# Kernel tuning notes

Hardware: AMD Instinct MI355X
Metric: run time of the kernel (lower is better)

## Reference

```python
import jax, jax.numpy as jnp
import numpy as np

BN_EPS = 1e-5
L2_EPS = 1e-12


def setup_inputs() -> dict:
    key = jax.random.key(0)
    k1, k2, k3 = jax.random.split(key, 3)
    B, N, D, K, G = 32, 2048, 512, 64, 16
    init_sc = 1.0 / np.sqrt(D)
    x = jax.random.normal(k1, (B, N, D), dtype=jnp.float32)
    clusters = init_sc * jax.random.normal(k2, (D, K + G), dtype=jnp.float32)
    clusters2 = init_sc * jax.random.normal(k3, (1, D, K), dtype=jnp.float32)
    bn_gamma = jnp.ones((K + G,), dtype=jnp.float32)
    bn_beta = jnp.zeros((K + G,), dtype=jnp.float32)
    return {"x": x, "clusters": clusters, "clusters2": clusters2,
            "bn_gamma": bn_gamma, "bn_beta": bn_beta}


def reference(x, clusters, clusters2, bn_gamma, bn_beta):
    B, N, D = x.shape
    K = clusters2.shape[-1]
    xf = x.reshape(B * N, D)
    # soft cluster assignment: [B*N, K+G]
    assn = xf @ clusters
    # BatchNorm1d (training-mode batch statistics, biased variance)
    mean = jnp.mean(assn, axis=0)
    var = jnp.var(assn, axis=0)
    assn = (assn - mean) * jax.lax.rsqrt(var + BN_EPS) * bn_gamma + bn_beta
    # softmax over clusters, then drop ghost clusters
    assn = jax.nn.softmax(assn, axis=1)[:, :K].reshape(B, N, K)
    # residual aggregation
    a_sum = jnp.sum(assn, axis=1, keepdims=True)          # [B, 1, K]
    a = a_sum * clusters2                                  # [B, D, K]
    vlad = jnp.einsum("bnk,bnd->bdk", assn, x) - a         # [B, D, K]
    # intra-normalization across feature dim D
    vlad = vlad / jnp.maximum(jnp.linalg.norm(vlad, axis=1, keepdims=True), L2_EPS)
    # flatten and global L2 normalization
    vlad = vlad.reshape(B, D * K)
    vlad = vlad / jnp.maximum(jnp.linalg.norm(vlad, axis=1, keepdims=True), L2_EPS)
    return vlad
```

## Files before the change

kernel.cpp:

```cpp
#include <hip/hip_runtime.h>
#include <hip/hip_bf16.h>
#include <stdint.h>

typedef __attribute__((ext_vector_type(8))) short short8;
typedef __attribute__((ext_vector_type(4))) float f32x4;

__device__ __forceinline__ float b2f(uint16_t u) {
  union { uint32_t i; float f; } v; v.i = ((uint32_t)u) << 16; return v.f;
}
__device__ __forceinline__ uint16_t f2b(float f) {
  uint32_t u = __float_as_uint(f);
  return (uint16_t)((u + 0x7FFFu + ((u >> 16) & 1u)) >> 16);
}
__device__ __forceinline__ uint32_t pk2(uint32_t lo, uint32_t hi) {
  return __builtin_amdgcn_perm(hi + 0x8000u, lo + 0x8000u, 0x07060302u);
}

__global__ void k0_prep(const float* __restrict__ clusters,
                        uint16_t* __restrict__ cB) {
  int gid = blockIdx.x * 256 + threadIdx.x;
  if (gid < 40960) {
    int i = gid & 7, chunk = gid >> 3;
    int lr = chunk & 15, q = (chunk >> 4) & 3, c5 = chunk >> 6;
    int n = c5 % 5, kk = c5 / 5;
    cB[gid] = f2b(clusters[(kk * 32 + q * 8 + i) * 80 + n * 16 + lr]);
  }
}

__global__ __launch_bounds__(256) void k1_gemm1(
    const float* __restrict__ x, const uint16_t* __restrict__ cB,
    float* __restrict__ raw, float* __restrict__ part) {
  __shared__ float sf[1280];
  const int t = threadIdx.x;
  const int w = t >> 6, lane = t & 63, q = lane >> 4, lr = lane & 15;
  const int rbase = blockIdx.x * 128 + w * 32;

  f32x4 acc[2][5];
#pragma unroll
  for (int m = 0; m < 2; ++m)
#pragma unroll
    for (int n = 0; n < 5; ++n) acc[m][n] = 0.f;

  const float* xa = x + (size_t)(rbase + lr) * 512 + q * 8;
  const short8* cbq = (const short8*)cB + q * 16 + lr;

#pragma unroll 2
  for (int kk = 0; kk < 16; ++kk) {
    short8 a[2], bf[5];
#pragma unroll
    for (int m = 0; m < 2; ++m) {
      uint4 u0 = *(const uint4*)(xa + (size_t)m * 16 * 512 + kk * 32);
      uint4 u1 = *(const uint4*)(xa + (size_t)m * 16 * 512 + kk * 32 + 4);
      union { short8 s; uint32_t u[4]; } av;
      av.u[0] = pk2(u0.x, u0.y); av.u[1] = pk2(u0.z, u0.w);
      av.u[2] = pk2(u1.x, u1.y); av.u[3] = pk2(u1.z, u1.w);
      a[m] = av.s;
    }
#pragma unroll
    for (int n = 0; n < 5; ++n)
      bf[n] = cbq[(kk * 5 + n) * 64];
#pragma unroll
    for (int m = 0; m < 2; ++m)
#pragma unroll
      for (int n = 0; n < 5; ++n)
        acc[m][n] = __builtin_amdgcn_mfma_f32_16x16x32_bf16(a[m], bf[n], acc[m][n], 0, 0, 0);
  }

  float sums[5], sqs[5];
#pragma unroll
  for (int n = 0; n < 5; ++n) {
    float s = 0.f, qq = 0.f;
#pragma unroll
    for (int m = 0; m < 2; ++m) {
#pragma unroll
      for (int r = 0; r < 4; ++r) {
        float v = acc[m][n][r];
        s += v; qq += v * v;
        raw[(size_t)(rbase + m * 16 + q * 4 + r) * 80 + n * 16 + lr] = v;
      }
    }
    s += __shfl_xor(s, 16);  s += __shfl_xor(s, 32);
    qq += __shfl_xor(qq, 16); qq += __shfl_xor(qq, 32);
    sums[n] = s; sqs[n] = qq;
  }

  if (lane < 16) {
#pragma unroll
    for (int n = 0; n < 5; ++n) {
      sf[w * 160 + n * 16 + lr] = sums[n];
      sf[640 + w * 160 + n * 16 + lr] = sqs[n];
    }
  }
  __syncthreads();
  if (t < 160) {
    float a0 = sf[t] + sf[160 + t] + sf[320 + t] + sf[480 + t];
    float b0 = sf[640 + t] + sf[800 + t] + sf[960 + t] + sf[1120 + t];
    part[(size_t)t * 512 + blockIdx.x] = a0;
    part[(size_t)(160 + t) * 512 + blockIdx.x] = b0;
  }
}

__global__ __launch_bounds__(64) void k2_stats(
    const float* __restrict__ part, const float* __restrict__ gamma,
    const float* __restrict__ beta, float* __restrict__ scsh) {
  int c = blockIdx.x, t = threadIdx.x;
  const float* p1 = part + (size_t)c * 512;
  const float* p2 = part + (size_t)(160 + c) * 512;
  float s1 = 0.f, s2 = 0.f;
#pragma unroll
  for (int p = 0; p < 512; p += 64) { s1 += p1[p + t]; s2 += p2[p + t]; }
#pragma unroll
  for (int o = 1; o < 64; o <<= 1) { s1 += __shfl_xor(s1, o); s2 += __shfl_xor(s2, o); }
  if (t == 0) {
    float mean = s1 * (1.f / 65536.f);
    float var = s2 * (1.f / 65536.f) - mean * mean;
    float sc = rsqrtf(var + 1e-5f) * gamma[c];
    scsh[c] = sc;
    scsh[80 + c] = beta[c] - mean * sc;
  }
}

__global__ __launch_bounds__(256, 2) void k34_fused(
    const float* __restrict__ x, const float* __restrict__ raw_,
    const float* __restrict__ scsh, float* __restrict__ vpart,
    float* __restrict__ apart) {
  __shared__ __align__(16) uint16_t sx[2][256 * 40];
  __shared__ __align__(16) uint16_t sp[2][64 * 40];
  __shared__ float sc[80], sh[80];
  __shared__ float ared[4 * 64];

  const int t = threadIdx.x;
  const int b = blockIdx.x >> 4;
  const int s = (blockIdx.x >> 1) & 7;
  const int dh = blockIdx.x & 1;
  const int w = t >> 6, lane = t & 63, q = lane >> 4, lr = lane & 15;

  const int dd = t;
  const int sg = ((dd >> 2) + (dd >> 4)) & 3;
  const int r_ = t >> 3, cg = t & 7;
  const int kk_ = t & 63, ng = t >> 6;

  if (t < 80) sc[t] = scsh[t];
  else if (t < 160) sh[t - 80] = scsh[t];

  const float* xb = x + ((size_t)b * 2048 + (size_t)s * 256) * 512 + dh * 256;
  const float* rawb = raw_ + ((size_t)b * 2048 + (size_t)s * 256) * 80;

  f32x4 acc[4][4];
#pragma unroll
  for (int m = 0; m < 4; ++m)
#pragma unroll
    for (int j = 0; j < 4; ++j) acc[m][j] = 0.f;

  float xf[32], yf[10];
  float asum = 0.f;

#define XLOAD(c)                                                          \
  {                                                                       \
    const float* xc = xb + (size_t)(c) * 32 * 512 + dd;                   \
    _Pragma("unroll")                                                     \
    for (int j = 0; j < 32; ++j) xf[j] = xc[(size_t)j * 512];             \
  }
#define RLOAD(c)                                                          \
  {                                                                       \
    const float* rc = rawb + (size_t)((c) * 32 + r_) * 80 + cg * 10;      \
    _Pragma("unroll")                                                     \
    for (int j = 0; j < 5; ++j) {                                         \
      float2 v2 = *(const float2*)(rc + j * 2);                           \
      yf[2 * j] = v2.x; yf[2 * j + 1] = v2.y;                             \
    }                                                                     \
  }
#define XSTORE(buf)                                                       \
  {                                                                       \
    _Pragma("unroll")                                                     \
    for (int g = 0; g < 4; ++g) {                                         \
      union { uint4 u; uint32_t w4[4]; } pv;                              \
      _Pragma("unroll")                                                   \
      for (int h = 0; h < 4; ++h)                                         \
        pv.w4[h] = pk2(__float_as_uint(xf[g * 8 + h * 2]),                \
                       __float_as_uint(xf[g * 8 + h * 2 + 1]));           \
      *(uint4*)&sx[buf][dd * 40 + ((g ^ sg) << 3)] = pv.u;                \
    }                                                                     \
  }
#define SOFTMAX(buf)                                                      \
  {                                                                       \
    float yy[10]; float mx = -3.0e38f;                                    \
    _Pragma("unroll")                                                     \
    for (int j = 0; j < 10; ++j) {                                        \
      int cc = cg * 10 + j;                                               \
      yy[j] = yf[j] * sc[cc] + sh[cc];                                    \
      mx = fmaxf(mx, yy[j]);                                              \
    }                                                                     \
    mx = fmaxf(mx, __shfl_xor(mx, 1));                                    \
    mx = fmaxf(mx, __shfl_xor(mx, 2));                                    \
    mx = fmaxf(mx, __shfl_xor(mx, 4));                                    \
    float sum = 0.f;                                                      \
    _Pragma("unroll")                                                     \
    for (int j = 0; j < 10; ++j) { yy[j] = __expf(yy[j] - mx); sum += yy[j]; } \
    sum += __shfl_xor(sum, 1);                                            \
    sum += __shfl_xor(sum, 2);                                            \
    sum += __shfl_xor(sum, 4);                                            \
    float inv = 1.0f / sum;                                               \
    _Pragma("unroll")                                                     \
    for (int j = 0; j < 10; ++j) {                                        \
      int cc = cg * 10 + j;                                               \
      if (cc < 64) sp[buf][cc * 40 + r_] = f2b(yy[j] * inv);              \
    }                                                                     \
  }
#define GEMM(buf)                                                         \
  {                                                                       \
    const uint16_t* sxc = sx[buf];                                        \
    const uint16_t* spc = sp[buf];                                        \
    short8 bfr[4];                                                        \
    _Pragma("unroll")                                                     \
    for (int j = 0; j < 4; ++j)                                           \
      bfr[j] = *(const short8*)&spc[(j * 16 + lr) * 40 + (q << 3)];       \
    _Pragma("unroll")                                                     \
    for (int m = 0; m < 4; ++m) {                                         \
      int row = w * 64 + m * 16 + lr;                                     \
      int swr = ((row >> 2) + (row >> 4)) & 3;                            \
      short8 af = *(const short8*)&sxc[row * 40 + ((q ^ swr) << 3)];      \
      _Pragma("unroll")                                                   \
      for (int j = 0; j < 4; ++j)                                         \
        acc[m][j] = __builtin_amdgcn_mfma_f32_16x16x32_bf16(af, bfr[j], acc[m][j], 0, 0, 0); \
    }                                                                     \
    union { uint4 u; uint16_t us[8]; } pv;                                \
    pv.u = *(const uint4*)&spc[kk_ * 40 + (ng << 3)];                     \
    _Pragma("unroll")                                                     \
    for (int i = 0; i < 8; ++i) asum += b2f(pv.us[i]);                    \
  }

  XLOAD(0) RLOAD(0)
  __syncthreads();
  XSTORE(0) SOFTMAX(0)
  XLOAD(1) RLOAD(1)
  __syncthreads();

  for (int c = 0; c < 8; ++c) {
    const int cur = c & 1;
    if (c < 7) {
      XSTORE(cur ^ 1) SOFTMAX(cur ^ 1)
      if (c < 6) { XLOAD(c + 2) RLOAD(c + 2) }
    }
    GEMM(cur)
    __syncthreads();
  }
#undef XLOAD
#undef RLOAD
#undef XSTORE
#undef SOFTMAX
#undef GEMM

  ared[ng * 64 + kk_] = asum;
  __syncthreads();
  if (dh == 0 && t < 64) {
    float a = ared[t] + ared[64 + t] + ared[128 + t] + ared[192 + t];
    apart[((size_t)b * 8 + s) * 64 + t] = a;
  }

  float* vp = vpart + ((size_t)s * 32 + b) * 32768;
#pragma unroll
  for (int m = 0; m < 4; ++m)
#pragma unroll
    for (int j = 0; j < 4; ++j)
#pragma unroll
      for (int r2 = 0; r2 < 4; ++r2)
        vp[(size_t)(dh * 256 + w * 64 + m * 16 + q * 4 + r2) * 64 + j * 16 + lr] =
            acc[m][j][r2];
}

__global__ __launch_bounds__(256) void k5a_red(
    const float* __restrict__ vpart, const float* __restrict__ apart,
    const float* __restrict__ c2, float* __restrict__ vfull,
    float* __restrict__ csq) {
  __shared__ float las[64];
  __shared__ float sred[16 * 64];
  const int t = threadIdx.x, b = blockIdx.x >> 4, dg = blockIdx.x & 15;
  if (t < 64) {
    float a = 0.f;
#pragma unroll
    for (int s = 0; s < 8; ++s) a += apart[((size_t)b * 8 + s) * 64 + t];
    las[t] = a;
  }
  __syncthreads();
  const int di = t >> 4, kq = t & 15;
  const float4 lasv = *(const float4*)&las[kq * 4];
  float4 ssq = {0.f, 0.f, 0.f, 0.f};
#pragma unroll
  for (int jj = 0; jj < 2; ++jj) {
    int d = dg * 32 + jj * 16 + di;
    size_t i = (size_t)d * 64 + kq * 4;
    float4 cc = *(const float4*)(c2 + i);
    float4 v;
    v.x = -lasv.x * cc.x; v.y = -lasv.y * cc.y;
    v.z = -lasv.z * cc.z; v.w = -lasv.w * cc.w;
#pragma unroll
    for (int s = 0; s < 8; ++s) {
      float4 p = *(const float4*)(vpart + ((size_t)s * 32 + b) * 32768 + i);
      v.x += p.x; v.y += p.y; v.z += p.z; v.w += p.w;
    }
    *(float4*)(vfull + (size_t)b * 32768 + i) = v;
    ssq.x += v.x * v.x; ssq.y += v.y * v.y;
    ssq.z += v.z * v.z; ssq.w += v.w * v.w;
  }
  *(float4*)&sred[di * 64 + kq * 4] = ssq;
  __syncthreads();
  if (t < 64) {
    float s0 = 0.f;
#pragma unroll
    for (int di2 = 0; di2 < 16; ++di2) s0 += sred[di2 * 64 + t];
    csq[(size_t)blockIdx.x * 64 + t] = s0;
  }
}

__global__ __launch_bounds__(64) void k5b_fin(
    const float* __restrict__ csq, float* __restrict__ linv,
    float* __restrict__ gscl) {
  const int t = threadIdx.x, b = blockIdx.x;
  float ssq = 0.f;
#pragma unroll
  for (int dg = 0; dg < 16; ++dg) ssq += csq[(size_t)(b * 16 + dg) * 64 + t];
  float iv = 1.0f / fmaxf(sqrtf(ssq), 1e-12f);
  linv[b * 64 + t] = iv;
  float contrib = ssq * iv * iv;
#pragma unroll
  for (int o = 1; o < 64; o <<= 1) contrib += __shfl_xor(contrib, o);
  if (t == 0) gscl[b] = 1.0f / fmaxf(sqrtf(contrib), 1e-12f);
}

__global__ __launch_bounds__(256) void k5c_norm(
    const float* __restrict__ vfull, const float* __restrict__ linv,
    const float* __restrict__ gscl, float* __restrict__ out) {
  __shared__ float lv[64];
  __shared__ float gs;
  const int t = threadIdx.x, b = blockIdx.x >> 4, seg = blockIdx.x & 15;
  if (t < 64) lv[t] = linv[b * 64 + t];
  if (t == 64) gs = gscl[b];
  __syncthreads();
  const float gg = gs;
#pragma unroll
  for (int u = 0; u < 2; ++u) {
    int i = seg * 2048 + u * 1024 + t * 4;
    int k0 = i & 63;
    float4 a = *(const float4*)(vfull + (size_t)b * 32768 + i);
    float4 o;
    o.x = a.x * lv[k0 + 0] * gg;
    o.y = a.y * lv[k0 + 1] * gg;
    o.z = a.z * lv[k0 + 2] * gg;
    o.w = a.w * lv[k0 + 3] * gg;
    *(float4*)&out[(size_t)b * 32768 + i] = o;
  }
}

extern "C" void kernel_launch(void* const* d_in, const int* in_sizes, int n_in,
                              void* d_out, int out_size, void* d_ws, size_t ws_size,
                              hipStream_t stream) {
  const float* x         = (const float*)d_in[0];
  const float* clusters  = (const float*)d_in[1];
  const float* clusters2 = (const float*)d_in[2];
  const float* gamma     = (const float*)d_in[3];
  const float* beta      = (const float*)d_in[4];
  float* out = (float*)d_out;
  char* ws = (char*)d_ws;

  uint16_t* cB = (uint16_t*)(ws + 0);
  float* part  = (float*)(ws + 81920);
  float* scsh  = (float*)(ws + 737280);
  float* raw   = (float*)(ws + 737920);
  float* vpart = (float*)(ws + 21709440);
  float* vfull = (float*)(ws + 55263872);
  float* apart = (float*)(ws + 59458176);
  float* csq   = (float*)(ws + 59523712);
  float* linv  = (float*)(ws + 59654784);
  float* gscl  = (float*)(ws + 59662976);

  hipLaunchKernelGGL(k0_prep,   dim3(160), dim3(256), 0, stream, clusters, cB);
  hipLaunchKernelGGL(k1_gemm1,  dim3(512), dim3(256), 0, stream, x, cB, raw, part);
  hipLaunchKernelGGL(k2_stats,  dim3(80),  dim3(64),  0, stream, part, gamma, beta, scsh);
  hipLaunchKernelGGL(k34_fused, dim3(512), dim3(256), 0, stream, x, raw, scsh, vpart, apart);
  hipLaunchKernelGGL(k5a_red,   dim3(512), dim3(256), 0, stream, vpart, apart, clusters2, vfull, csq);
  hipLaunchKernelGGL(k5b_fin,   dim3(32),  dim3(64),  0, stream, csq, linv, gscl);
  hipLaunchKernelGGL(k5c_norm,  dim3(512), dim3(256), 0, stream, vfull, linv, gscl, out);
}
```

Before: 249.6 us.

## Halve GEMM1 rows per block, software-pipeline loads, fold k5b into k5c

The assignment GEMM kernel now gives each wave 16 rows instead of 32 and doubles the grid to 1024 blocks. It asks for occupancy 4 and fully unrolls the K loop, prefetching x two steps ahead and the cluster fragments one step ahead. The aim is to raise memory-level parallelism and hide load latency in a kernel bound by reading x. The per-cluster norm finalisation kernel is merged into the final normalisation kernel to drop one launch, at the cost of each of the 16 blocks per batch recomputing the same norms.

```diff
diff --git a/kernel.cpp b/kernel.cpp
--- a/kernel.cpp
+++ b/kernel.cpp
@@ -27,43 +27,47 @@
   }
 }
 
-__global__ __launch_bounds__(256) void k1_gemm1(
+__global__ __launch_bounds__(256, 4) void k1_gemm1(
     const float* __restrict__ x, const uint16_t* __restrict__ cB,
     float* __restrict__ raw, float* __restrict__ part) {
   __shared__ float sf[1280];
   const int t = threadIdx.x;
   const int w = t >> 6, lane = t & 63, q = lane >> 4, lr = lane & 15;
-  const int rbase = blockIdx.x * 128 + w * 32;
-
-  f32x4 acc[2][5];
-#pragma unroll
-  for (int m = 0; m < 2; ++m)
-#pragma unroll
-    for (int n = 0; n < 5; ++n) acc[m][n] = 0.f;
+  const int rbase = blockIdx.x * 64 + w * 16;
+
+  f32x4 acc[5];
+#pragma unroll
+  for (int n = 0; n < 5; ++n) acc[n] = 0.f;
 
   const float* xa = x + (size_t)(rbase + lr) * 512 + q * 8;
   const short8* cbq = (const short8*)cB + q * 16 + lr;
 
-#pragma unroll 2
+  uint4 u0[2], u1[2];
+  u0[0] = *(const uint4*)(xa);          u1[0] = *(const uint4*)(xa + 4);
+  u0[1] = *(const uint4*)(xa + 32);     u1[1] = *(const uint4*)(xa + 36);
+  short8 bfc[5], bfp[5];
+#pragma unroll
+  for (int n = 0; n < 5; ++n) bfc[n] = cbq[n * 64];
+
+#pragma unroll
   for (int kk = 0; kk < 16; ++kk) {
-    short8 a[2], bf[5];
-#pragma unroll
-    for (int m = 0; m < 2; ++m) {
-      uint4 u0 = *(const uint4*)(xa + (size_t)m * 16 * 512 + kk * 32);
-      uint4 u1 = *(const uint4*)(xa + (size_t)m * 16 * 512 + kk * 32 + 4);
-      union { short8 s; uint32_t u[4]; } av;
-      av.u[0] = pk2(u0.x, u0.y); av.u[1] = pk2(u0.z, u0.w);
-      av.u[2] = pk2(u1.x, u1.y); av.u[3] = pk2(u1.z, u1.w);
-      a[m] = av.s;
+    const int si = kk & 1;
+    union { short8 s; uint32_t u[4]; } av;
+    av.u[0] = pk2(u0[si].x, u0[si].y); av.u[1] = pk2(u0[si].z, u0[si].w);
+    av.u[2] = pk2(u1[si].x, u1[si].y); av.u[3] = pk2(u1[si].z, u1[si].w);
+    if (kk < 15) {
+#pragma unroll
+      for (int n = 0; n < 5; ++n) bfp[n] = cbq[((kk + 1) * 5 + n) * 64];
+    }
+    if (kk < 14) {
+      u0[si] = *(const uint4*)(xa + (kk + 2) * 32);
+      u1[si] = *(const uint4*)(xa + (kk + 2) * 32 + 4);
     }
 #pragma unroll
     for (int n = 0; n < 5; ++n)
-      bf[n] = cbq[(kk * 5 + n) * 64];
-#pragma unroll
-    for (int m = 0; m < 2; ++m)
-#pragma unroll
-      for (int n = 0; n < 5; ++n)
-        acc[m][n] = __builtin_amdgcn_mfma_f32_16x16x32_bf16(a[m], bf[n], acc[m][n], 0, 0, 0);
+      acc[n] = __builtin_amdgcn_mfma_f32_16x16x32_bf16(av.s, bfc[n], acc[n], 0, 0, 0);
+#pragma unroll
+    for (int n = 0; n < 5; ++n) bfc[n] = bfp[n];
   }
 
   float sums[5], sqs[5];
@@ -71,13 +75,10 @@
   for (int n = 0; n < 5; ++n) {
     float s = 0.f, qq = 0.f;
 #pragma unroll
-    for (int m = 0; m < 2; ++m) {
-#pragma unroll
-      for (int r = 0; r < 4; ++r) {
-        float v = acc[m][n][r];
-        s += v; qq += v * v;
-        raw[(size_t)(rbase + m * 16 + q * 4 + r) * 80 + n * 16 + lr] = v;
-      }
+    for (int r = 0; r < 4; ++r) {
+      float v = acc[n][r];
+      s += v; qq += v * v;
+      raw[(size_t)(rbase + q * 4 + r) * 80 + n * 16 + lr] = v;
     }
     s += __shfl_xor(s, 16);  s += __shfl_xor(s, 32);
     qq += __shfl_xor(qq, 16); qq += __shfl_xor(qq, 32);
@@ -95,8 +96,8 @@
   if (t < 160) {
     float a0 = sf[t] + sf[160 + t] + sf[320 + t] + sf[480 + t];
     float b0 = sf[640 + t] + sf[800 + t] + sf[960 + t] + sf[1120 + t];
-    part[(size_t)t * 512 + blockIdx.x] = a0;
-    part[(size_t)(160 + t) * 512 + blockIdx.x] = b0;
+    part[(size_t)t * 1024 + blockIdx.x] = a0;
+    part[(size_t)(160 + t) * 1024 + blockIdx.x] = b0;
   }
 }
 
@@ -104,11 +105,11 @@
     const float* __restrict__ part, const float* __restrict__ gamma,
     const float* __restrict__ beta, float* __restrict__ scsh) {
   int c = blockIdx.x, t = threadIdx.x;
-  const float* p1 = part + (size_t)c * 512;
-  const float* p2 = part + (size_t)(160 + c) * 512;
+  const float* p1 = part + (size_t)c * 1024;
+  const float* p2 = part + (size_t)(160 + c) * 1024;
   float s1 = 0.f, s2 = 0.f;
 #pragma unroll
-  for (int p = 0; p < 512; p += 64) { s1 += p1[p + t]; s2 += p2[p + t]; }
+  for (int p = 0; p < 1024; p += 64) { s1 += p1[p + t]; s2 += p2[p + t]; }
 #pragma unroll
   for (int o = 1; o < 64; o <<= 1) { s1 += __shfl_xor(s1, o); s2 += __shfl_xor(s2, o); }
   if (t == 0) {
@@ -313,31 +314,25 @@
   }
 }
 
-__global__ __launch_bounds__(64) void k5b_fin(
-    const float* __restrict__ csq, float* __restrict__ linv,
-    float* __restrict__ gscl) {
-  const int t = threadIdx.x, b = blockIdx.x;
-  float ssq = 0.f;
-#pragma unroll
-  for (int dg = 0; dg < 16; ++dg) ssq += csq[(size_t)(b * 16 + dg) * 64 + t];
-  float iv = 1.0f / fmaxf(sqrtf(ssq), 1e-12f);
-  linv[b * 64 + t] = iv;
-  float contrib = ssq * iv * iv;
-#pragma unroll
-  for (int o = 1; o < 64; o <<= 1) contrib += __shfl_xor(contrib, o);
-  if (t == 0) gscl[b] = 1.0f / fmaxf(sqrtf(contrib), 1e-12f);
-}
-
 __global__ __launch_bounds__(256) void k5c_norm(
-    const float* __restrict__ vfull, const float* __restrict__ linv,
-    const float* __restrict__ gscl, float* __restrict__ out) {
+    const float* __restrict__ csq, const float* __restrict__ vfull,
+    float* __restrict__ out) {
   __shared__ float lv[64];
-  __shared__ float gs;
+  __shared__ float gsv;
   const int t = threadIdx.x, b = blockIdx.x >> 4, seg = blockIdx.x & 15;
-  if (t < 64) lv[t] = linv[b * 64 + t];
-  if (t == 64) gs = gscl[b];
-  __syncthreads();
-  const float gg = gs;
+  if (t < 64) {
+    float ssq = 0.f;
+#pragma unroll
+    for (int dg = 0; dg < 16; ++dg) ssq += csq[(size_t)(b * 16 + dg) * 64 + t];
+    float iv = 1.0f / fmaxf(sqrtf(ssq), 1e-12f);
+    lv[t] = iv;
+    float contrib = ssq * iv * iv;
+#pragma unroll
+    for (int o = 1; o < 64; o <<= 1) contrib += __shfl_xor(contrib, o);
+    if (t == 0) gsv = 1.0f / fmaxf(sqrtf(contrib), 1e-12f);
+  }
+  __syncthreads();
+  const float gg = gsv;
 #pragma unroll
   for (int u = 0; u < 2; ++u) {
     int i = seg * 2048 + u * 1024 + t * 4;
@@ -365,20 +360,17 @@
 
   uint16_t* cB = (uint16_t*)(ws + 0);
   float* part  = (float*)(ws + 81920);
-  float* scsh  = (float*)(ws + 737280);
-  float* raw   = (float*)(ws + 737920);
-  float* vpart = (float*)(ws + 21709440);
-  float* vfull = (float*)(ws + 55263872);
-  float* apart = (float*)(ws + 59458176);
-  float* csq   = (float*)(ws + 59523712);
-  float* linv  = (float*)(ws + 59654784);
-  float* gscl  = (float*)(ws + 59662976);
-
-  hipLaunchKernelGGL(k0_prep,   dim3(160), dim3(256), 0, stream, clusters, cB);
-  hipLaunchKernelGGL(k1_gemm1,  dim3(512), dim3(256), 0, stream, x, cB, raw, part);
-  hipLaunchKernelGGL(k2_stats,  dim3(80),  dim3(64),  0, stream, part, gamma, beta, scsh);
-  hipLaunchKernelGGL(k34_fused, dim3(512), dim3(256), 0, stream, x, raw, scsh, vpart, apart);
-  hipLaunchKernelGGL(k5a_red,   dim3(512), dim3(256), 0, stream, vpart, apart, clusters2, vfull, csq);
-  hipLaunchKernelGGL(k5b_fin,   dim3(32),  dim3(64),  0, stream, csq, linv, gscl);
-  hipLaunchKernelGGL(k5c_norm,  dim3(512), dim3(256), 0, stream, vfull, linv, gscl, out);
-}
+  float* scsh  = (float*)(ws + 1392640);
+  float* raw   = (float*)(ws + 1393280);
+  float* vpart = (float*)(ws + 22364800);
+  float* vfull = (float*)(ws + 55919232);
+  float* apart = (float*)(ws + 60113536);
+  float* csq   = (float*)(ws + 60179072);
+
+  hipLaunchKernelGGL(k0_prep,   dim3(160),  dim3(256), 0, stream, clusters, cB);
+  hipLaunchKernelGGL(k1_gemm1,  dim3(1024), dim3(256), 0, stream, x, cB, raw, part);
+  hipLaunchKernelGGL(k2_stats,  dim3(80),   dim3(64),  0, stream, part, gamma, beta, scsh);
+  hipLaunchKernelGGL(k34_fused, dim3(512),  dim3(256), 0, stream, x, raw, scsh, vpart, apart);
+  hipLaunchKernelGGL(k5a_red,   dim3(512),  dim3(256), 0, stream, vpart, apart, clusters2, vfull, csq);
+  hipLaunchKernelGGL(k5c_norm,  dim3(512),  dim3(256), 0, stream, csq, vfull, out);
+}
```

Result: no change. 250.3 us (+0.3%).
